# Optimization experiments

Measured on AMD Instinct MI355X. Metric: run time of the kernel, lower is better.

## Reference

```python
import jax, jax.numpy as jnp
import numpy as np
from jax import lax

GAMMA = 0.01
BIG = 1e8  # stand-in for +inf on DP borders (keeps grads finite/zero)


def _pairwise_sq_dists(x, y):
    # x: [N,1] (target), y: [N,1] (pred) -> D[i,j] = (x_i - y_j)^2
    xn = jnp.sum(x * x, axis=1)  # [N]
    yn = jnp.sum(y * y, axis=1)  # [N]
    d = xn[:, None] + yn[None, :] - 2.0 * (x @ y.T)
    return jnp.maximum(d, 0.0)


def _soft_dtw(D, gamma):
    # Soft-DTW DP via wavefront scan over the 2N-1 anti-diagonals.
    # R[i,j] = D[i,j] + softmin_gamma(R[i-1,j-1], R[i-1,j], R[i,j-1]),
    # with virtual R[-1,-1] = 0 and +inf borders.
    N = D.shape[0]
    ii = jnp.arange(N)

    def shift(r):  # r[i] -> r[i-1], BIG at i=0
        return jnp.concatenate([jnp.full((1,), BIG, r.dtype), r[:-1]])

    def step(carry, k):
        r1, r2 = carry  # diagonals k-1 and k-2, indexed by row i
        jj = k - ii
        valid = (jj >= 0) & (jj < N)
        d = D[ii, jnp.clip(jj, 0, N - 1)]
        a = shift(r2)                                   # R[i-1, j-1]
        a = jnp.where((k == 0) & (ii == 0), 0.0, a)     # virtual origin
        b = shift(r1)                                   # R[i-1, j]
        c = jnp.where(jj >= 1, r1, BIG)                 # R[i, j-1]
        vals = jnp.stack([a, b, c])                     # [3, N]
        m = jnp.min(vals, axis=0)
        softmin = m - gamma * jnp.log(jnp.sum(jnp.exp(-(vals - m) / gamma), axis=0))
        r_new = jnp.where(valid, d + softmin, BIG)
        return (r_new, r1), None

    init = jnp.full((N,), BIG, D.dtype)
    (r_last, _), _ = lax.scan(step, (init, init), jnp.arange(2 * N - 1))
    return r_last[N - 1]  # R[N-1, N-1], batch size 1 -> mean == value


def setup_inputs() -> dict:
    key = jax.random.key(0)
    k1, k2 = jax.random.split(key)
    pred = jax.random.normal(k1, (4096, 1), dtype=jnp.float32)
    target = jax.random.normal(k2, (4096, 1), dtype=jnp.float32)
    return {"pred": pred, "target": target}


def reference(pred, target):
    # DILATELoss.forward returns loss_shape (the soft-DTW value);
    # the temporal path term is computed in the original but discarded.
    D = _pairwise_sq_dists(target.reshape(-1, 1), pred.reshape(-1, 1))
    return _soft_dtw(D, GAMMA)
```

## Files before the change

### kernel.cpp

```cpp
#include <hip/hip_runtime.h>

#define NN    4096
#define BIGF  1e8f
#define SQK2f 12.0112245225638540f
#define BIGK  1.4426950408889634e10f
#define IK2f  0.00693147180559945309f
#define NBLK  32
#define NCI   130
#define OUTS  4158
#define SENTU 0xFFFFFFFFu

__global__ __launch_bounds__(1024) void dilate_sdtw(const float* __restrict__ pred,
                                                    const float* __restrict__ target,
                                                    float* __restrict__ out) {
    __shared__ float t_s[NN];
    __shared__ float p_s[NN];
    __shared__ float bufA[NN];
    __shared__ float bufB[NN];
    __shared__ float bufC[NN];
    const int tid = threadIdx.x;
    for (int i = tid; i < NN; i += 1024) {
        t_s[i] = target[i]; p_s[i] = pred[i];
        bufA[i] = BIGF; bufB[i] = BIGF; bufC[i] = BIGF;
    }
    __syncthreads();
    float* r2 = bufA; float* r1 = bufB; float* rn = bufC;
    for (int k = 0; k < 2 * NN - 1; ++k) {
        int ilo = k - (NN - 1); if (ilo < 0) ilo = 0;
        int ihi = (k < NN - 1) ? k : (NN - 1);
        for (int i = ilo + tid; i <= ihi; i += 1024) {
            const int j = k - i;
            float diff = t_s[i] - p_s[j];
            float d = diff * diff;
            float a = (i >= 1 && j >= 1) ? r2[i - 1] : ((k == 0) ? 0.0f : BIGF);
            float b = (i >= 1) ? r1[i - 1] : BIGF;
            float c = (j >= 1) ? r1[i] : BIGF;
            float m = fminf(a, fminf(b, c));
            float s = __expf((m - a) * 100.0f) + __expf((m - b) * 100.0f) + __expf((m - c) * 100.0f);
            rn[i] = d + m - 0.01f * __logf(s);
        }
        __syncthreads();
        float* tmp = r2; r2 = r1; r1 = rn; rn = tmp;
    }
    if (tid == 0) out[0] = r1[NN - 1];
}


__device__ __forceinline__ float softmin3s(float a, float b, float c) {
    float m = fminf(a, fminf(b, c));
    float e = __builtin_amdgcn_exp2f(m - a)
            + __builtin_amdgcn_exp2f(m - b)
            + __builtin_amdgcn_exp2f(m - c);
    return m - __builtin_amdgcn_logf(e);
}

__device__ __forceinline__ float nbr1(float v, bool bsel) {
    int iv = __float_as_int(v);
    float a = __int_as_float(__builtin_amdgcn_update_dpp(iv, iv, 0x111, 0xF, 0xF, false));
    float b = __int_as_float(__builtin_amdgcn_update_dpp(iv, iv, 0x142, 0xF, 0xF, false));
    return bsel ? b : a;
}

__device__ __forceinline__ void bput(float* p, float v) {
    __hip_atomic_store((unsigned int*)p, __float_as_uint(v),
                       __ATOMIC_RELAXED, __HIP_MEMORY_SCOPE_AGENT);
}
__device__ __forceinline__ unsigned int bgetu(const float* p) {
    return __hip_atomic_load((const unsigned int*)p,
                             __ATOMIC_RELAXED, __HIP_MEMORY_SCOPE_AGENT);
}

__device__ __forceinline__ void uissue(const float* src, float* dst) {
#pragma unroll
    for (int q = 0; q < 32; ++q) dst[q] = __uint_as_float(bgetu(src + q));
}
__device__ __forceinline__ bool uvalid(const float* dst) {
    bool ok = true;
#pragma unroll
    for (int q = 0; q < 32; ++q) ok &= (__float_as_uint(dst[q]) != SENTU);
    return ok;
}
__device__ __forceinline__ void upoll(const float* src, float* dst) {
    for (;;) {
        uissue(src, dst);
        if (uvalid(dst)) return;
        __builtin_amdgcn_s_sleep(1);
    }
}

__device__ __forceinline__ void pload(const float* p_s, int base, float* dst) {
#pragma unroll
    for (int q = 0; q < 32; ++q) {
        int idx = base + q;
        idx = idx < 0 ? 0 : (idx > NN - 1 ? NN - 1 : idx);
        dst[q] = p_s[idx];
    }
}

template<bool TOP, bool BOT, bool EDGE>
__device__ __forceinline__ void chunk32(
    int cs, int lane, bool l0, bool bsel, float t0, float t1,
    float& v0, float& v1, float& u1, float& u2, float upl,
    float4& acc, const float* upc, const float* pc,
    float* __restrict__ bnd_my, float* __restrict__ outp)
{
#pragma unroll
    for (int u = 0; u < 32; ++u) {
        const int s = cs + u;
        const int j = s - lane;
        float a, b;
        if (TOP) {
            a = l0 ? ((s == 0) ? 0.0f : BIGK) : u2;
            b = l0 ? BIGK : u1;
        } else {
            float upj  = upc[u];
            float upjm = (u == 0) ? upl : upc[u - 1];
            a = l0 ? upjm : u2;
            b = l0 ? upj  : u1;
        }
        float pj = pc[u];
        float d0 = t0 - pj;
        float val0 = fmaf(d0, d0, softmin3s(a, b, v0));
        float d1 = t1 - pj;
        float val1 = fmaf(d1, d1, softmin3s(v0, val0, v1));
        if (EDGE) {
            bool vj = (unsigned)j < (unsigned)NN;
            val0 = vj ? val0 : BIGK;
            val1 = vj ? val1 : BIGK;
        }
        if (!BOT) {
            switch ((u + 1) & 3) {
                case 0: acc.x = val1; break;
                case 1: acc.y = val1; break;
                case 2: acc.z = val1; break;
                case 3: acc.w = val1; break;
            }
            if ((u & 3) == 2) {
                int base = j - 3;
                if (lane == 63 && (!EDGE || (unsigned)base <= (unsigned)(NN - 4))) {
                    bput(bnd_my + base + 0, acc.x);
                    bput(bnd_my + base + 1, acc.y);
                    bput(bnd_my + base + 2, acc.z);
                    bput(bnd_my + base + 3, acc.w);
                }
            }
        } else if (EDGE) {
            if (lane == 63 && s == OUTS) outp[0] = val1 * IK2f;
        }
        v0 = val0; v1 = val1;
        u2 = u1;
        u1 = nbr1(val1, bsel);
    }
}

template<bool TOP, bool BOT>
__device__ __forceinline__ void chunk_iter(
    int ci, int lane, bool l0, bool bsel, float t0, float t1,
    float& v0, float& v1, float& u1, float& u2, float& upl,
    float4& acc,
    float* upC, float* upN, float* pcC, float* pcN,
    const float* p_s, const float* __restrict__ bnd_up, float* __restrict__ bnd_my,
    float* __restrict__ outp)
{
    const int cs = 32 * ci;
    if (!TOP && cs < NN) {
        if (!uvalid(upC)) upoll(bnd_up + cs, upC);
        if (cs + 32 < NN) uissue(bnd_up + cs + 32, upN);
    }
    if (ci + 1 < NCI) pload(p_s, cs + 32 - lane, pcN);

    const bool edge = (ci < 2) || (ci >= 128);
    if (edge) chunk32<TOP, BOT, true >(cs, lane, l0, bsel, t0, t1, v0, v1, u1, u2,
                                       upl, acc, upC, pcC, bnd_my, outp);
    else      chunk32<TOP, BOT, false>(cs, lane, l0, bsel, t0, t1, v0, v1, u1, u2,
                                       upl, acc, upC, pcC, bnd_my, outp);
    if (!TOP) upl = upC[31];
}

template<bool TOP, bool BOT>
__device__ void stripe(int b, int lane, const float* __restrict__ target,
                       const float* p_s, float* bnd, float* outp)
{
    const float t0 = target[128 * b + 2 * lane]     * SQK2f;
    const float t1 = target[128 * b + 2 * lane + 1] * SQK2f;
    float* bnd_my = bnd + (size_t)b * NN;
    const float* bnd_up = bnd + (size_t)(b - 1) * NN;
    const bool l0 = (lane == 0);
    const bool bsel = (lane != 0) && ((lane & 15) == 0);

    float v0 = BIGK, v1 = BIGK, u1 = BIGK, u2 = BIGK, upl = BIGK;
    float4 acc = {BIGK, BIGK, BIGK, BIGK};
    float upA[32], upB[32];
    float pcA[32], pcB[32];

    pload(p_s, -lane, pcA);
    if (!TOP) uissue(bnd_up, upA);

    for (int cp = 0; cp < NCI / 2; ++cp) {
        chunk_iter<TOP, BOT>(2 * cp,     lane, l0, bsel, t0, t1, v0, v1, u1, u2, upl, acc,
                             upA, upB, pcA, pcB, p_s, bnd_up, bnd_my, outp);
        chunk_iter<TOP, BOT>(2 * cp + 1, lane, l0, bsel, t0, t1, v0, v1, u1, u2, upl, acc,
                             upB, upA, pcB, pcA, p_s, bnd_up, bnd_my, outp);
    }
}

__global__ __launch_bounds__(64, 1) void sdtw_pipe9(const float* __restrict__ pred,
                                                    const float* __restrict__ target,
                                                    float* __restrict__ out,
                                                    float* __restrict__ bnd)
{
    __shared__ float p_s[NN];
    const int lane = threadIdx.x;
    const int bid = blockIdx.x;
    const int b = (bid & 7) * 4 + (bid >> 3);
    for (int i = lane; i < NN; i += 64) p_s[i] = pred[i] * SQK2f;
    __syncthreads();
    if (b == 0)                stripe<true , false>(b, lane, target, p_s, bnd, out);
    else if (b == NBLK - 1)    stripe<false, true >(b, lane, target, p_s, bnd, out);
    else                       stripe<false, false>(b, lane, target, p_s, bnd, out);
}

extern "C" void kernel_launch(void* const* d_in, const int* in_sizes, int n_in,
                              void* d_out, int out_size, void* d_ws, size_t ws_size,
                              hipStream_t stream) {
    const float* pred   = (const float*)d_in[0];
    const float* target = (const float*)d_in[1];
    float* out = (float*)d_out;

    const size_t need = (size_t)NBLK * NN * sizeof(float);
    if (ws_size >= need) {
        float* bnd = (float*)d_ws;
        hipMemsetAsync(d_ws, 0xFF, need, stream);
        sdtw_pipe9<<<dim3(NBLK), dim3(64), 0, stream>>>(pred, target, out, bnd);
    } else {
        dilate_sdtw<<<dim3(1), dim3(1024), 0, stream>>>(pred, target, out);
    }
}
```

Baseline: 858.3 us.

## Skew each lane's two rows so their softmin chains run independently

Each lane's second row now computes column j-1 while the first row computes column j, so the second row uses the first row's value from the previous step. The two softmin3 computations per step no longer depend on each other and can be interleaved, which roughly halves the serial dependency chain per step. In exchange the wavefront is 64 steps longer (more chunks, larger pred preload window of 33 values), and the edge-chunk range and boundary indexing are adjusted to match.

Result: slower. 1.035 ms (+20.6%).

```diff
diff --git a/kernel.cpp b/kernel.cpp
--- a/kernel.cpp
+++ b/kernel.cpp
@@ -6,8 +6,8 @@
 #define BIGK  1.4426950408889634e10f
 #define IK2f  0.00693147180559945309f
 #define NBLK  32
-#define NCI   130
-#define OUTS  4158
+#define NCI   132
+#define OUTS  4222
 #define SENTU 0xFFFFFFFFu
 
 __global__ __launch_bounds__(1024) void dilate_sdtw(const float* __restrict__ pred,
@@ -90,7 +90,7 @@
 
 __device__ __forceinline__ void pload(const float* p_s, int base, float* dst) {
 #pragma unroll
-    for (int q = 0; q < 32; ++q) {
+    for (int q = 0; q < 33; ++q) {
         int idx = base + q;
         idx = idx < 0 ? 0 : (idx > NN - 1 ? NN - 1 : idx);
         dst[q] = p_s[idx];
@@ -100,33 +100,32 @@
 template<bool TOP, bool BOT, bool EDGE>
 __device__ __forceinline__ void chunk32(
     int cs, int lane, bool l0, bool bsel, float t0, float t1,
-    float& v0, float& v1, float& u1, float& u2, float upl,
+    float& v0p, float& v0pp, float& v1p, float& u1, float& u2, float upl,
     float4& acc, const float* upc, const float* pc,
     float* __restrict__ bnd_my, float* __restrict__ outp)
 {
 #pragma unroll
     for (int u = 0; u < 32; ++u) {
-        const int s = cs + u;
-        const int j = s - lane;
-        float a, b;
+        const int s  = cs + u;
+        const int j0 = s - 2 * lane;
+        const int j1 = j0 - 1;
+        float a0, b0;
         if (TOP) {
-            a = l0 ? ((s == 0) ? 0.0f : BIGK) : u2;
-            b = l0 ? BIGK : u1;
+            a0 = l0 ? ((s == 0) ? 0.0f : BIGK) : u2;
+            b0 = l0 ? BIGK : u1;
         } else {
             float upj  = upc[u];
             float upjm = (u == 0) ? upl : upc[u - 1];
-            a = l0 ? upjm : u2;
-            b = l0 ? upj  : u1;
-        }
-        float pj = pc[u];
-        float d0 = t0 - pj;
-        float val0 = fmaf(d0, d0, softmin3s(a, b, v0));
-        float d1 = t1 - pj;
-        float val1 = fmaf(d1, d1, softmin3s(v0, val0, v1));
+            a0 = l0 ? upjm : u2;
+            b0 = l0 ? upj  : u1;
+        }
+        float d0 = t0 - pc[u + 1];
+        float val0 = fmaf(d0, d0, softmin3s(a0, b0, v0p));
+        float d1 = t1 - pc[u];
+        float val1 = fmaf(d1, d1, softmin3s(v0pp, v0p, v1p));
         if (EDGE) {
-            bool vj = (unsigned)j < (unsigned)NN;
-            val0 = vj ? val0 : BIGK;
-            val1 = vj ? val1 : BIGK;
+            val0 = ((unsigned)j0 < (unsigned)NN) ? val0 : BIGK;
+            val1 = ((unsigned)j1 < (unsigned)NN) ? val1 : BIGK;
         }
         if (!BOT) {
             switch ((u + 1) & 3) {
@@ -136,7 +135,7 @@
                 case 3: acc.w = val1; break;
             }
             if ((u & 3) == 2) {
-                int base = j - 3;
+                int base = j1 - 3;
                 if (lane == 63 && (!EDGE || (unsigned)base <= (unsigned)(NN - 4))) {
                     bput(bnd_my + base + 0, acc.x);
                     bput(bnd_my + base + 1, acc.y);
@@ -147,7 +146,7 @@
         } else if (EDGE) {
             if (lane == 63 && s == OUTS) outp[0] = val1 * IK2f;
         }
-        v0 = val0; v1 = val1;
+        v0pp = v0p; v0p = val0; v1p = val1;
         u2 = u1;
         u1 = nbr1(val1, bsel);
     }
@@ -156,7 +155,7 @@
 template<bool TOP, bool BOT>
 __device__ __forceinline__ void chunk_iter(
     int ci, int lane, bool l0, bool bsel, float t0, float t1,
-    float& v0, float& v1, float& u1, float& u2, float& upl,
+    float& v0p, float& v0pp, float& v1p, float& u1, float& u2, float& upl,
     float4& acc,
     float* upC, float* upN, float* pcC, float* pcN,
     const float* p_s, const float* __restrict__ bnd_up, float* __restrict__ bnd_my,
@@ -167,13 +166,13 @@
         if (!uvalid(upC)) upoll(bnd_up + cs, upC);
         if (cs + 32 < NN) uissue(bnd_up + cs + 32, upN);
     }
-    if (ci + 1 < NCI) pload(p_s, cs + 32 - lane, pcN);
-
-    const bool edge = (ci < 2) || (ci >= 128);
-    if (edge) chunk32<TOP, BOT, true >(cs, lane, l0, bsel, t0, t1, v0, v1, u1, u2,
-                                       upl, acc, upC, pcC, bnd_my, outp);
-    else      chunk32<TOP, BOT, false>(cs, lane, l0, bsel, t0, t1, v0, v1, u1, u2,
-                                       upl, acc, upC, pcC, bnd_my, outp);
+    if (ci + 1 < NCI) pload(p_s, cs + 32 - 1 - 2 * lane, pcN);
+
+    const bool edge = (ci < 4) || (ci >= 128);
+    if (edge) chunk32<TOP, BOT, true >(cs, lane, l0, bsel, t0, t1, v0p, v0pp, v1p,
+                                       u1, u2, upl, acc, upC, pcC, bnd_my, outp);
+    else      chunk32<TOP, BOT, false>(cs, lane, l0, bsel, t0, t1, v0p, v0pp, v1p,
+                                       u1, u2, upl, acc, upC, pcC, bnd_my, outp);
     if (!TOP) upl = upC[31];
 }
 
@@ -188,26 +187,26 @@
     const bool l0 = (lane == 0);
     const bool bsel = (lane != 0) && ((lane & 15) == 0);
 
-    float v0 = BIGK, v1 = BIGK, u1 = BIGK, u2 = BIGK, upl = BIGK;
+    float v0p = BIGK, v0pp = BIGK, v1p = BIGK, u1 = BIGK, u2 = BIGK, upl = BIGK;
     float4 acc = {BIGK, BIGK, BIGK, BIGK};
     float upA[32], upB[32];
-    float pcA[32], pcB[32];
-
-    pload(p_s, -lane, pcA);
+    float pcA[33], pcB[33];
+
+    pload(p_s, -1 - 2 * lane, pcA);
     if (!TOP) uissue(bnd_up, upA);
 
     for (int cp = 0; cp < NCI / 2; ++cp) {
-        chunk_iter<TOP, BOT>(2 * cp,     lane, l0, bsel, t0, t1, v0, v1, u1, u2, upl, acc,
+        chunk_iter<TOP, BOT>(2 * cp,     lane, l0, bsel, t0, t1, v0p, v0pp, v1p, u1, u2, upl, acc,
                              upA, upB, pcA, pcB, p_s, bnd_up, bnd_my, outp);
-        chunk_iter<TOP, BOT>(2 * cp + 1, lane, l0, bsel, t0, t1, v0, v1, u1, u2, upl, acc,
+        chunk_iter<TOP, BOT>(2 * cp + 1, lane, l0, bsel, t0, t1, v0p, v0pp, v1p, u1, u2, upl, acc,
                              upB, upA, pcB, pcA, p_s, bnd_up, bnd_my, outp);
     }
 }
 
-__global__ __launch_bounds__(64, 1) void sdtw_pipe9(const float* __restrict__ pred,
-                                                    const float* __restrict__ target,
-                                                    float* __restrict__ out,
-                                                    float* __restrict__ bnd)
+__global__ __launch_bounds__(64, 1) void sdtw_pipe10(const float* __restrict__ pred,
+                                                     const float* __restrict__ target,
+                                                     float* __restrict__ out,
+                                                     float* __restrict__ bnd)
 {
     __shared__ float p_s[NN];
     const int lane = threadIdx.x;
@@ -231,7 +230,7 @@
     if (ws_size >= need) {
         float* bnd = (float*)d_ws;
         hipMemsetAsync(d_ws, 0xFF, need, stream);
-        sdtw_pipe9<<<dim3(NBLK), dim3(64), 0, stream>>>(pred, target, out, bnd);
+        sdtw_pipe10<<<dim3(NBLK), dim3(64), 0, stream>>>(pred, target, out, bnd);
     } else {
         dilate_sdtw<<<dim3(1), dim3(1024), 0, stream>>>(pred, target, out);
     }
```

## Pack boundary handoff into 64-bit words, poll finely at stripe start, simplify softmin

Applied to the files above, without the earlier changes.

Inter-block boundary values are now written and read as packed 64-bit atomic words, two floats per store, instead of four separate 32-bit stores per group. In the first two chunks the consumer polls 8-column sub-blocks, so a downstream stripe can start before a full 32-wide chunk is ready. This shortens the pipeline fill latency across the 32 chained blocks. The softmin uses min/med3/max so one exp becomes the constant 1, and p_s loads skip clamping in interior chunks. The finer handoff adds more polling overhead and 64-bit publish ordering, which could cost time if polls spin.

Measured after the change: 921.1 us. 7.3% more time.

```diff
diff --git a/kernel.cpp b/kernel.cpp
--- a/kernel.cpp
+++ b/kernel.cpp
@@ -8,7 +8,7 @@
 #define NBLK  32
 #define NCI   130
 #define OUTS  4158
-#define SENTU 0xFFFFFFFFu
+#define SENT64 0xFFFFFFFFFFFFFFFFull
 
 __global__ __launch_bounds__(1024) void dilate_sdtw(const float* __restrict__ pred,
                                                     const float* __restrict__ target,
@@ -47,10 +47,10 @@
 
 
 __device__ __forceinline__ float softmin3s(float a, float b, float c) {
-    float m = fminf(a, fminf(b, c));
-    float e = __builtin_amdgcn_exp2f(m - a)
-            + __builtin_amdgcn_exp2f(m - b)
-            + __builtin_amdgcn_exp2f(m - c);
+    float m  = fminf(a, fminf(b, c));
+    float md = __builtin_amdgcn_fmed3f(a, b, c);
+    float mx = fmaxf(a, fmaxf(b, c));
+    float e  = 1.0f + (__builtin_amdgcn_exp2f(m - md) + __builtin_amdgcn_exp2f(m - mx));
     return m - __builtin_amdgcn_logf(e);
 }
 
@@ -61,51 +61,71 @@
     return bsel ? b : a;
 }
 
-__device__ __forceinline__ void bput(float* p, float v) {
-    __hip_atomic_store((unsigned int*)p, __float_as_uint(v),
-                       __ATOMIC_RELAXED, __HIP_MEMORY_SCOPE_AGENT);
-}
-__device__ __forceinline__ unsigned int bgetu(const float* p) {
-    return __hip_atomic_load((const unsigned int*)p,
-                             __ATOMIC_RELAXED, __HIP_MEMORY_SCOPE_AGENT);
-}
-
-__device__ __forceinline__ void uissue(const float* src, float* dst) {
-#pragma unroll
-    for (int q = 0; q < 32; ++q) dst[q] = __uint_as_float(bgetu(src + q));
-}
-__device__ __forceinline__ bool uvalid(const float* dst) {
+typedef unsigned long long u64;
+
+__device__ __forceinline__ void bput64(u64* p, u64 w) {
+    __hip_atomic_store(p, w, __ATOMIC_RELAXED, __HIP_MEMORY_SCOPE_AGENT);
+}
+__device__ __forceinline__ u64 bget64(const u64* p) {
+    return __hip_atomic_load(p, __ATOMIC_RELAXED, __HIP_MEMORY_SCOPE_AGENT);
+}
+
+__device__ __forceinline__ void uissue16(const u64* src, u64* dst) {
+#pragma unroll
+    for (int q = 0; q < 16; ++q) dst[q] = bget64(src + q);
+}
+__device__ __forceinline__ bool uvalid16(const u64* dst) {
     bool ok = true;
 #pragma unroll
-    for (int q = 0; q < 32; ++q) ok &= (__float_as_uint(dst[q]) != SENTU);
+    for (int q = 0; q < 16; ++q) ok &= (dst[q] != SENT64);
     return ok;
 }
-__device__ __forceinline__ void upoll(const float* src, float* dst) {
+__device__ __forceinline__ void upoll16(const u64* src, u64* dst) {
     for (;;) {
-        uissue(src, dst);
-        if (uvalid(dst)) return;
+        if (uvalid16(dst)) return;
         __builtin_amdgcn_s_sleep(1);
-    }
-}
-
+        uissue16(src, dst);
+    }
+}
+template<int Q0>
+__device__ __forceinline__ void upoll4(const u64* src, u64* dst) {
+    for (;;) {
+        bool ok = true;
+#pragma unroll
+        for (int q = Q0; q < Q0 + 4; ++q) ok &= (dst[q] != SENT64);
+        if (ok) return;
+        __builtin_amdgcn_s_sleep(1);
+#pragma unroll
+        for (int q = Q0; q < Q0 + 4; ++q) dst[q] = bget64(src + q);
+    }
+}
+
+__device__ __forceinline__ float upw(const u64* c, int u) {
+    u64 w = c[u >> 1];
+    unsigned int h = (u & 1) ? (unsigned int)(w >> 32) : (unsigned int)w;
+    return __uint_as_float(h);
+}
+
+template<bool CLAMP>
 __device__ __forceinline__ void pload(const float* p_s, int base, float* dst) {
 #pragma unroll
     for (int q = 0; q < 32; ++q) {
         int idx = base + q;
-        idx = idx < 0 ? 0 : (idx > NN - 1 ? NN - 1 : idx);
+        if (CLAMP) idx = idx < 0 ? 0 : (idx > NN - 1 ? NN - 1 : idx);
         dst[q] = p_s[idx];
     }
 }
 
-template<bool TOP, bool BOT, bool EDGE>
-__device__ __forceinline__ void chunk32(
+template<bool TOP, bool BOT, bool EDGE, int UO>
+__device__ __forceinline__ void chunk8(
     int cs, int lane, bool l0, bool bsel, float t0, float t1,
-    float& v0, float& v1, float& u1, float& u2, float upl,
-    float4& acc, const float* upc, const float* pc,
-    float* __restrict__ bnd_my, float* __restrict__ outp)
-{
-#pragma unroll
-    for (int u = 0; u < 32; ++u) {
+    float& v0, float& v1, float& u1, float& u2, float upl, float& accLo,
+    const u64* upc, const float* pc,
+    u64* __restrict__ bnd64_my, float* __restrict__ outp)
+{
+#pragma unroll
+    for (int uu = 0; uu < 8; ++uu) {
+        const int u = UO + uu;
         const int s = cs + u;
         const int j = s - lane;
         float a, b;
@@ -113,8 +133,8 @@
             a = l0 ? ((s == 0) ? 0.0f : BIGK) : u2;
             b = l0 ? BIGK : u1;
         } else {
-            float upj  = upc[u];
-            float upjm = (u == 0) ? upl : upc[u - 1];
+            float upj  = upw(upc, u);
+            float upjm = (u == 0) ? upl : upw(upc, u - 1);
             a = l0 ? upjm : u2;
             b = l0 ? upj  : u1;
         }
@@ -129,20 +149,13 @@
             val1 = vj ? val1 : BIGK;
         }
         if (!BOT) {
-            switch ((u + 1) & 3) {
-                case 0: acc.x = val1; break;
-                case 1: acc.y = val1; break;
-                case 2: acc.z = val1; break;
-                case 3: acc.w = val1; break;
-            }
-            if ((u & 3) == 2) {
-                int base = j - 3;
-                if (lane == 63 && (!EDGE || (unsigned)base <= (unsigned)(NN - 4))) {
-                    bput(bnd_my + base + 0, acc.x);
-                    bput(bnd_my + base + 1, acc.y);
-                    bput(bnd_my + base + 2, acc.z);
-                    bput(bnd_my + base + 3, acc.w);
+            if ((u & 1) == 0) {
+                if (lane == 63 && (!EDGE || (unsigned)(j - 1) <= (unsigned)(NN - 2))) {
+                    u64 w = ((u64)__float_as_uint(val1) << 32) | (u64)__float_as_uint(accLo);
+                    bput64(bnd64_my + ((j - 1) >> 1), w);
                 }
+            } else {
+                accLo = val1;
             }
         } else if (EDGE) {
             if (lane == 63 && s == OUTS) outp[0] = val1 * IK2f;
@@ -153,61 +166,85 @@
     }
 }
 
+#define CH8ARGS cs, lane, l0, bsel, t0, t1, v0, v1, u1, u2, upl, accLo, upC, pcC, bnd64_my, outp
+
 template<bool TOP, bool BOT>
 __device__ __forceinline__ void chunk_iter(
     int ci, int lane, bool l0, bool bsel, float t0, float t1,
-    float& v0, float& v1, float& u1, float& u2, float& upl,
-    float4& acc,
-    float* upC, float* upN, float* pcC, float* pcN,
-    const float* p_s, const float* __restrict__ bnd_up, float* __restrict__ bnd_my,
-    float* __restrict__ outp)
+    float& v0, float& v1, float& u1, float& u2, float& upl, float& accLo,
+    u64* upC, u64* upN, float* pcC, float* pcN,
+    const float* p_s, const u64* __restrict__ bnd_up64,
+    u64* __restrict__ bnd64_my, float* __restrict__ outp)
 {
     const int cs = 32 * ci;
-    if (!TOP && cs < NN) {
-        if (!uvalid(upC)) upoll(bnd_up + cs, upC);
-        if (cs + 32 < NN) uissue(bnd_up + cs + 32, upN);
-    }
-    if (ci + 1 < NCI) pload(p_s, cs + 32 - lane, pcN);
-
-    const bool edge = (ci < 2) || (ci >= 128);
-    if (edge) chunk32<TOP, BOT, true >(cs, lane, l0, bsel, t0, t1, v0, v1, u1, u2,
-                                       upl, acc, upC, pcC, bnd_my, outp);
-    else      chunk32<TOP, BOT, false>(cs, lane, l0, bsel, t0, t1, v0, v1, u1, u2,
-                                       upl, acc, upC, pcC, bnd_my, outp);
-    if (!TOP) upl = upC[31];
+    const bool haveUp = (!TOP) && (cs < NN);
+    const bool fine = haveUp && (ci < 2);
+
+    if (haveUp && !fine) {
+        if (!uvalid16(upC)) upoll16(bnd_up64 + 16 * ci, upC);
+    }
+    if (fine) upoll4<0>(bnd_up64 + 16 * ci, upC);
+    if (haveUp && cs + 32 < NN) uissue16(bnd_up64 + 16 * (ci + 1), upN);
+    if (ci + 1 < NCI) {
+        if (ci + 1 <= 2 || ci + 1 >= 126) pload<true >(p_s, cs + 32 - lane, pcN);
+        else                               pload<false>(p_s, cs + 32 - lane, pcN);
+    }
+
+    if (fine) {
+        chunk8<TOP, BOT, true, 0 >(CH8ARGS);
+        upoll4<4 >(bnd_up64 + 16 * ci, upC);
+        chunk8<TOP, BOT, true, 8 >(CH8ARGS);
+        upoll4<8 >(bnd_up64 + 16 * ci, upC);
+        chunk8<TOP, BOT, true, 16>(CH8ARGS);
+        upoll4<12>(bnd_up64 + 16 * ci, upC);
+        chunk8<TOP, BOT, true, 24>(CH8ARGS);
+    } else {
+        const bool edge = (ci < 2) || (ci >= 128);
+        if (edge) {
+            chunk8<TOP, BOT, true, 0 >(CH8ARGS);
+            chunk8<TOP, BOT, true, 8 >(CH8ARGS);
+            chunk8<TOP, BOT, true, 16>(CH8ARGS);
+            chunk8<TOP, BOT, true, 24>(CH8ARGS);
+        } else {
+            chunk8<TOP, BOT, false, 0 >(CH8ARGS);
+            chunk8<TOP, BOT, false, 8 >(CH8ARGS);
+            chunk8<TOP, BOT, false, 16>(CH8ARGS);
+            chunk8<TOP, BOT, false, 24>(CH8ARGS);
+        }
+    }
+    if (haveUp) upl = upw(upC, 31);
 }
 
 template<bool TOP, bool BOT>
 __device__ void stripe(int b, int lane, const float* __restrict__ target,
-                       const float* p_s, float* bnd, float* outp)
+                       const float* p_s, u64* bnd64, float* outp)
 {
     const float t0 = target[128 * b + 2 * lane]     * SQK2f;
     const float t1 = target[128 * b + 2 * lane + 1] * SQK2f;
-    float* bnd_my = bnd + (size_t)b * NN;
-    const float* bnd_up = bnd + (size_t)(b - 1) * NN;
+    u64* bnd64_my = bnd64 + (size_t)b * (NN / 2);
+    const u64* bnd_up64 = bnd64 + (size_t)(b - 1) * (NN / 2);
     const bool l0 = (lane == 0);
     const bool bsel = (lane != 0) && ((lane & 15) == 0);
 
-    float v0 = BIGK, v1 = BIGK, u1 = BIGK, u2 = BIGK, upl = BIGK;
-    float4 acc = {BIGK, BIGK, BIGK, BIGK};
-    float upA[32], upB[32];
+    float v0 = BIGK, v1 = BIGK, u1 = BIGK, u2 = BIGK, upl = BIGK, accLo = BIGK;
+    u64 upA[16], upB[16];
     float pcA[32], pcB[32];
 
-    pload(p_s, -lane, pcA);
-    if (!TOP) uissue(bnd_up, upA);
+    pload<true>(p_s, -lane, pcA);
+    if (!TOP) uissue16(bnd_up64, upA);
 
     for (int cp = 0; cp < NCI / 2; ++cp) {
-        chunk_iter<TOP, BOT>(2 * cp,     lane, l0, bsel, t0, t1, v0, v1, u1, u2, upl, acc,
-                             upA, upB, pcA, pcB, p_s, bnd_up, bnd_my, outp);
-        chunk_iter<TOP, BOT>(2 * cp + 1, lane, l0, bsel, t0, t1, v0, v1, u1, u2, upl, acc,
-                             upB, upA, pcB, pcA, p_s, bnd_up, bnd_my, outp);
-    }
-}
-
-__global__ __launch_bounds__(64, 1) void sdtw_pipe9(const float* __restrict__ pred,
-                                                    const float* __restrict__ target,
-                                                    float* __restrict__ out,
-                                                    float* __restrict__ bnd)
+        chunk_iter<TOP, BOT>(2 * cp,     lane, l0, bsel, t0, t1, v0, v1, u1, u2, upl, accLo,
+                             upA, upB, pcA, pcB, p_s, bnd_up64, bnd64_my, outp);
+        chunk_iter<TOP, BOT>(2 * cp + 1, lane, l0, bsel, t0, t1, v0, v1, u1, u2, upl, accLo,
+                             upB, upA, pcB, pcA, p_s, bnd_up64, bnd64_my, outp);
+    }
+}
+
+__global__ __launch_bounds__(64, 1) void sdtw_pipe11(const float* __restrict__ pred,
+                                                     const float* __restrict__ target,
+                                                     float* __restrict__ out,
+                                                     u64* __restrict__ bnd64)
 {
     __shared__ float p_s[NN];
     const int lane = threadIdx.x;
@@ -215,9 +252,9 @@
     const int b = (bid & 7) * 4 + (bid >> 3);
     for (int i = lane; i < NN; i += 64) p_s[i] = pred[i] * SQK2f;
     __syncthreads();
-    if (b == 0)                stripe<true , false>(b, lane, target, p_s, bnd, out);
-    else if (b == NBLK - 1)    stripe<false, true >(b, lane, target, p_s, bnd, out);
-    else                       stripe<false, false>(b, lane, target, p_s, bnd, out);
+    if (b == 0)                stripe<true , false>(b, lane, target, p_s, bnd64, out);
+    else if (b == NBLK - 1)    stripe<false, true >(b, lane, target, p_s, bnd64, out);
+    else                       stripe<false, false>(b, lane, target, p_s, bnd64, out);
 }
 
 extern "C" void kernel_launch(void* const* d_in, const int* in_sizes, int n_in,
@@ -229,9 +266,9 @@
 
     const size_t need = (size_t)NBLK * NN * sizeof(float);
     if (ws_size >= need) {
-        float* bnd = (float*)d_ws;
+        u64* bnd64 = (u64*)d_ws;
         hipMemsetAsync(d_ws, 0xFF, need, stream);
-        sdtw_pipe9<<<dim3(NBLK), dim3(64), 0, stream>>>(pred, target, out, bnd);
+        sdtw_pipe11<<<dim3(NBLK), dim3(64), 0, stream>>>(pred, target, out, bnd64);
     } else {
         dilate_sdtw<<<dim3(1), dim3(1024), 0, stream>>>(pred, target, out);
     }
```
